# Performance work log

Measured on AMD Instinct MI355X. Metric: run time of the kernel, lower is better.

The kernel has to match this reference:

```python
import jax, jax.numpy as jnp
import numpy as np

D_MODEL = 512
NUM_HEADS = 8
WINDOW = 10
DEPTH = D_MODEL // NUM_HEADS


def positional_encoding(position, d_model):
    pos = np.arange(position)[:, None].astype(np.float32)
    i = np.arange(d_model)[None, :].astype(np.float32)
    angle = pos / np.power(10000.0, 2.0 * (np.floor(i / 2.0)) / np.float32(d_model))
    angle[:, 0::2] = np.sin(angle[:, 0::2])
    angle[:, 1::2] = np.cos(angle[:, 1::2])
    return jnp.asarray(angle[None, ...], dtype=jnp.float32)  # [1, n, d_model]


def forward(x, wq_w, wq_b, wk_w, wk_b, wv_w, wv_b, dense_w, dense_b):
    B, C, S, _ = x.shape
    data = x[..., 0]
    mask = x[..., 2]
    data = data.reshape(B, C, -1, WINDOW)   # [B,C,n,W]
    mask = mask.reshape(B, C, -1, WINDOW)
    n = data.shape[2]

    # mean_module: (data*mask).mean over window, drop first/last window
    mean_feature = jnp.mean(data * mask, axis=-1, keepdims=True)[:, :, 1:-1]  # [B,C,n-2,1]

    # combined look-ahead + padding mask
    mask_min = jnp.min(mask[:, :, 1:-1], axis=-1)              # [B,C,n-2]
    n2 = n - 2
    look_ahead = 1.0 - jnp.tril(jnp.ones((n2, n2), jnp.float32))
    padding = (mask_min == 0).astype(jnp.float32)[:, :, None, None, :]  # [B,C,1,1,n-2]
    comb_mask = jnp.maximum(look_ahead, padding)               # [B,C,1,n-2,n-2]

    # positional encoding over window dimension
    pe = positional_encoding(n, WINDOW)                        # [1,n,W]
    data = data + pe[None]                                     # [B,C,n,W]

    # q,k from concatenated future/past windows; v from current windows
    qk_in = jnp.concatenate([data[:, :, 2:], data[:, :, :-2]], axis=-1)  # [B,C,n-2,2W]
    q = qk_in @ wq_w + wq_b
    k = qk_in @ wk_w + wk_b
    v = data[:, :, 1:-1] @ wv_w + wv_b                          # [B,C,n-2,d_model]

    def split_heads(t):
        return t.reshape(B, C, n2, NUM_HEADS, DEPTH).transpose(0, 1, 3, 2, 4)

    q, k, v = split_heads(q), split_heads(k), split_heads(v)    # [B,C,H,n-2,depth]

    logits = jnp.einsum('bchqd,bchkd->bchqk', q, k) / jnp.sqrt(jnp.float32(DEPTH))
    logits = logits + comb_mask * (-1e9)
    attn = jax.nn.softmax(logits, axis=-1)
    ctx = jnp.einsum('bchqk,bchkd->bchqd', attn, v)
    ctx = ctx.transpose(0, 1, 3, 2, 4).reshape(B, C, n2, D_MODEL)

    concat = jnp.concatenate([ctx, mean_feature], axis=-1)      # [B,C,n-2,d_model+1]
    out = concat @ dense_w + dense_b                            # [B,C,n-2,W]
    return out.reshape(B, C, -1)[..., None]                     # [B,C,(n-2)*W,1]


def setup_inputs() -> dict:
    key = jax.random.key(0)
    ks = jax.random.split(key, 8)
    B, C, S = 16, 16, 2560
    data = jax.random.normal(ks[0], (B, C, S), jnp.float32)
    time = jnp.zeros((B, C, S), jnp.float32)
    mask = (jax.random.uniform(ks[1], (B, C, S)) < 0.9).astype(jnp.float32)
    x = jnp.stack([data, time, mask], axis=-1)
    scale = 0.02
    return {
        'x': x,
        'wq_w': jax.random.normal(ks[2], (2 * WINDOW, D_MODEL), jnp.float32) * scale,
        'wq_b': jnp.zeros((D_MODEL,), jnp.float32),
        'wk_w': jax.random.normal(ks[3], (2 * WINDOW, D_MODEL), jnp.float32) * scale,
        'wk_b': jnp.zeros((D_MODEL,), jnp.float32),
        'wv_w': jax.random.normal(ks[4], (WINDOW, D_MODEL), jnp.float32) * scale,
        'wv_b': jnp.zeros((D_MODEL,), jnp.float32),
        'dense_w': jax.random.normal(ks[5], (D_MODEL + 1, WINDOW), jnp.float32) * scale,
        'dense_b': jnp.zeros((WINDOW,), jnp.float32),
    }


def reference(x, wq_w, wq_b, wk_w, wk_b, wv_w, wv_b, dense_w, dense_b):
    return forward(x, wq_w, wq_b, wk_w, wk_b, wv_w, wv_b, dense_w, dense_b)
```

## Files before the change

kernel.cpp:

```cpp
#include <hip/hip_runtime.h>

#define LOG2E 1.44269504088896340736f
#define SCL 0.18033688011111772f

typedef __bf16 bf16x8 __attribute__((ext_vector_type(8)));
typedef float f32x16 __attribute__((ext_vector_type(16)));

union U4B { uint4 u; bf16x8 v; };

static __device__ __forceinline__ unsigned short f2bf(float f) {
  unsigned u = __builtin_bit_cast(unsigned, f);
  u += 0x7FFFu + ((u >> 16) & 1u);
  return (unsigned short)(u >> 16);
}
static __device__ __forceinline__ float bf2f(unsigned short s) {
  unsigned u = ((unsigned)s) << 16;
  return __builtin_bit_cast(float, u);
}
static __device__ __forceinline__ f32x16 zero16() {
  f32x16 z;
#pragma unroll
  for (int i = 0; i < 16; ++i) z[i] = 0.f;
  return z;
}
static __device__ __forceinline__ f32x16 MFMA(bf16x8 a, bf16x8 b, f32x16 c) {
  return __builtin_amdgcn_mfma_f32_32x32x16_bf16(a, b, c, 0, 0, 0);
}

static __device__ __forceinline__ void xform(f32x16 t, int hi, uint4& f0, uint4& f1) {
  unsigned pk[8], sw[8];
#pragma unroll
  for (int s = 0; s < 8; ++s) {
    unsigned d;
    asm("v_cvt_pk_bf16_f32 %0, %1, %2" : "=v"(d) : "v"(t[2*s]), "v"(t[2*s+1]));
    pk[s] = d;
  }
#pragma unroll
  for (int s = 0; s < 8; ++s) sw[s] = (unsigned)__shfl_xor((int)pk[s], 32);
  if (hi) {
    f0 = make_uint4(sw[2], sw[3], pk[2], pk[3]);
    f1 = make_uint4(sw[6], sw[7], pk[6], pk[7]);
  } else {
    f0 = make_uint4(pk[0], pk[1], sw[0], sw[1]);
    f1 = make_uint4(pk[4], pk[5], sw[4], sw[5]);
  }
}

__global__ void zero_out_k(float* __restrict__ out, int n) {
  int i = blockIdx.x * 256 + threadIdx.x;
  if (i < n) out[i] = 0.f;
}

__global__ void setup_k(
    const float* __restrict__ wq_w, const float* __restrict__ wq_b,
    const float* __restrict__ wk_w, const float* __restrict__ wk_b,
    const float* __restrict__ wv_w, const float* __restrict__ wv_b,
    const float* __restrict__ dense_w, float* __restrict__ ws)
{
  int gid = blockIdx.x*256 + threadIdx.x;
  float* pe = ws;
  unsigned short* wqT = (unsigned short*)(ws + 2560);
  unsigned short* wkT = (unsigned short*)(ws + 10752);
  float* WVD = ws + 18944;
  float* bvd = ws + 19744;
  if (gid < 2560) {
    int i = gid/10, t = gid%10;
    double ex = (double)(2*(t/2)) / 10.0;
    double ang = (double)i * pow(10000.0, -ex);
    pe[gid] = (float)((t & 1) ? cos(ang) : sin(ang));
  } else if (gid < 2560 + 16384) {
    int idx = gid - 2560;
    int hd = idx >> 5, t = idx & 31;
    float v = (t < 20) ? wq_w[t*512 + hd] : ((t == 20) ? wq_b[hd] : 0.f);
    wqT[idx] = f2bf(v);
  } else if (gid < 2560 + 32768) {
    int idx = gid - (2560 + 16384);
    int hd = idx >> 5, t = idx & 31;
    float v = (t < 20) ? wk_w[t*512 + hd] : ((t == 20) ? wk_b[hd] : 0.f);
    wkT[idx] = f2bf(v);
  } else if (gid < 2560 + 32768 + 800) {
    int idx = gid - (2560 + 32768);
    int h = idx/100, rem = idx%100, t = rem/10, w = rem%10;
    float s = 0.f;
    for (int d = 0; d < 64; ++d) s += wv_w[t*512 + h*64 + d] * dense_w[(h*64 + d)*10 + w];
    WVD[idx] = s;
  } else if (gid < 2560 + 32768 + 880) {
    int idx = gid - (2560 + 32768 + 800);
    int h = idx/10, w = idx%10;
    float s = 0.f;
    for (int d = 0; d < 64; ++d) s += wv_b[h*64 + d] * dense_w[(h*64 + d)*10 + w];
    bvd[idx] = s;
  }
}

__global__ __launch_bounds__(256, 1) void mha_fused(
    const float* __restrict__ x,
    const float* __restrict__ dense_w, const float* __restrict__ dense_b,
    const unsigned short* __restrict__ wqT, const unsigned short* __restrict__ wkT,
    const float* __restrict__ WVD, const float* __restrict__ bvd,
    const float* __restrict__ pe,
    float* __restrict__ out)
{
  __shared__ __align__(16) unsigned short qk_in[256*24];
  __shared__ __align__(16) unsigned short k_lds[256*64];
  __shared__ __align__(16) unsigned short vdT[16*256];
  __shared__ unsigned short mean_b[256];
  __shared__ unsigned long long padb[4];
  __shared__ float ddmean_s[10];

  const int tid = threadIdx.x;
  const int lane = tid & 63;
  const int wv = tid >> 6;
  const int hi = lane >> 5;
  const int cc = lane & 31;
  const int bc = blockIdx.x / 3;
  const int p3 = blockIdx.x - bc*3;
  const int hbase = p3*3;
  const int nh = (p3 == 2) ? 2 : 3;

  float ddr[10];
  {
    const float* xb = x + ((size_t)bc*2560 + tid*10)*3;
    float dat[10], msk[10];
#pragma unroll
    for (int t = 0; t < 10; ++t) { dat[t] = xb[3*t]; msk[t] = xb[3*t+2]; }
    float mean = 0.f, mm = msk[0];
#pragma unroll
    for (int t = 0; t < 10; ++t) { mean += dat[t]*msk[t]; mm = fminf(mm, msk[t]); }
    mean_b[tid] = f2bf(mean * 0.1f);
    const float* per = pe + tid*10;
#pragma unroll
    for (int t = 0; t < 10; ++t) ddr[t] = dat[t] + per[t];
    float* ddtmp = (float*)k_lds;
    float* mmv = ddtmp + 2560;
#pragma unroll
    for (int t = 0; t < 10; ++t) ddtmp[tid*10 + t] = ddr[t];
    mmv[tid] = mm;
  }
  __syncthreads();
  {
    const float* ddtmp = (const float*)k_lds;
    const float* mmv = ddtmp + 2560;
    float* part = (float*)vdT;
    if (tid < 254) {
#pragma unroll
      for (int t = 0; t < 10; ++t) qk_in[tid*24 + t] = f2bf(ddtmp[(tid+2)*10 + t]);
#pragma unroll
      for (int t = 0; t < 10; ++t) qk_in[tid*24 + 10 + t] = f2bf(ddr[t]);
      qk_in[tid*24 + 20] = 0x3F80;
      qk_in[tid*24 + 21] = 0; qk_in[tid*24 + 22] = 0; qk_in[tid*24 + 23] = 0;
    } else {
#pragma unroll
      for (int t = 0; t < 24; ++t) qk_in[tid*24 + t] = 0;
    }
    if (tid < 160) {
      int t = tid >> 4, j = tid & 15;
      int w0 = 1 + j*16, w1 = (w0 + 16 < 255) ? (w0 + 16) : 255;
      float s = 0.f;
      for (int w = w0; w < w1; ++w) s += ddtmp[w*10 + t];
      part[tid] = s;
    }
#pragma unroll
    for (int i = 0; i < 6; ++i) vdT[(10 + i)*256 + tid] = 0;
    bool cond = (tid >= 254) || (mmv[tid+1] == 0.0f);
    unsigned long long bl = __ballot(cond);
    if (lane == 0) padb[wv] = bl;
  }
  __syncthreads();
  if (tid < 10) {
    const float* part = (const float*)vdT;
    float s = 0.f;
#pragma unroll
    for (int j = 0; j < 16; ++j) s += part[tid*16 + j];
    ddmean_s[tid] = s * (1.0f/254.0f);
  }
  float dwcol = 0.f, dbias = 0.f;
  if (cc < 10) { dwcol = dense_w[5120 + cc]; dbias = dense_b[cc]; }
  const unsigned* pw = (const unsigned*)padb;

  f32x16 outacc0 = zero16(), outacc1 = zero16();

#pragma unroll 1
  for (int hh = 0; hh < nh; ++hh) {
    const int h = hbase + hh;
    __syncthreads();
    if (tid < 254) {
      float df[10];
      int src = tid + 1;
      if (src <= 253) {
#pragma unroll
        for (int t = 0; t < 10; ++t) df[t] = bf2f(qk_in[src*24 + 10 + t]);
      } else {
#pragma unroll
        for (int t = 0; t < 10; ++t) df[t] = bf2f(qk_in[252*24 + t]);
      }
      const float* wvd = WVD + h*100;
      const float* bv = bvd + h*10;
#pragma unroll
      for (int w = 0; w < 10; ++w) {
        float s = bv[w];
#pragma unroll
        for (int t = 0; t < 10; ++t) s += df[t]*wvd[t*10 + w];
        vdT[w*256 + (tid ^ ((w & 15)*8))] = f2bf(s);
      }
    }
    if (tid < 32) {
      int w = tid >> 1, j = 254 + (tid & 1);
      vdT[w*256 + (j ^ ((w & 15)*8))] = 0;
    }
    float mvd = 0.f;
    if (cc < 10) {
      mvd = bvd[h*10 + cc];
#pragma unroll
      for (int t = 0; t < 10; ++t) mvd = fmaf(ddmean_s[t], WVD[h*100 + t*10 + cc], mvd);
    }
    __syncthreads();

#pragma unroll
    for (int jti = 0; jti < 2; ++jti) {
      int jt = wv + 4*jti;
      int krow = 32*jt + cc;
      U4B b0, b1;
      b0.u = *(const uint4*)&qk_in[krow*24 + 8*hi];
      b1.u = make_uint4(0,0,0,0);
      if (!hi) b1.u = *(const uint4*)&qk_in[krow*24 + 16];
#pragma unroll
      for (int it = 0; it < 2; ++it) {
        const unsigned short* wrow = wkT + (h*64 + 32*it + cc)*32;
        U4B a0, a1;
        a0.u = *(const uint4*)&wrow[8*hi];
        a1.u = *(const uint4*)&wrow[16 + 8*hi];
        f32x16 acc = zero16();
        acc = MFMA(a0.v, b0.v, acc);
        acc = MFMA(a1.v, b1.v, acc);
        uint4 f0, f1;
        xform(acc, hi, f0, f1);
        int dc0 = 2*it, dc1 = 2*it + 1;
        *(uint4*)&k_lds[krow*64 + ((8*(2*dc0 + hi)) ^ (8*(krow & 7)))] = f0;
        *(uint4*)&k_lds[krow*64 + ((8*(2*dc1 + hi)) ^ (8*(krow & 7)))] = f1;
      }
    }
    __syncthreads();

#pragma unroll
    for (int qti = 0; qti < 2; ++qti) {
      const int qt = qti ? (7 - wv) : wv;
      const int qrow = 32*qt + cc;
      uint4 qf0, qf1, qf2, qf3;
      {
        U4B b0, b1;
        b0.u = *(const uint4*)&qk_in[qrow*24 + 8*hi];
        b1.u = make_uint4(0,0,0,0);
        if (!hi) b1.u = *(const uint4*)&qk_in[qrow*24 + 16];
        {
          const unsigned short* wrow = wqT + (h*64 + cc)*32;
          U4B a0, a1;
          a0.u = *(const uint4*)&wrow[8*hi];
          a1.u = *(const uint4*)&wrow[16 + 8*hi];
          f32x16 acc = zero16();
          acc = MFMA(a0.v, b0.v, acc);
          acc = MFMA(a1.v, b1.v, acc);
          xform(acc, hi, qf0, qf1);
        }
        {
          const unsigned short* wrow = wqT + (h*64 + 32 + cc)*32;
          U4B a0, a1;
          a0.u = *(const uint4*)&wrow[8*hi];
          a1.u = *(const uint4*)&wrow[16 + 8*hi];
          f32x16 acc = zero16();
          acc = MFMA(a0.v, b0.v, acc);
          acc = MFMA(a1.v, b1.v, acc);
          xform(acc, hi, qf2, qf3);
        }
      }
      float sum = 0.f;
      f32x16 pv = zero16();
      const int vrow = cc & 15;
      const int vsw = 8*vrow;
#pragma unroll
      for (int kt = 0; kt < 8; ++kt) {
        if (kt <= qt) {
          const int kr = 32*kt + cc;
          const int kbase = kr*64;
          const int ksw = 8*(kr & 7);
          f32x16 a = zero16();
          U4B ka, qa;
          ka.u = *(const uint4*)&k_lds[kbase + ((8*(0 + hi)) ^ ksw)];
          qa.u = qf0; a = MFMA(ka.v, qa.v, a);
          ka.u = *(const uint4*)&k_lds[kbase + ((8*(2 + hi)) ^ ksw)];
          qa.u = qf1; a = MFMA(ka.v, qa.v, a);
          ka.u = *(const uint4*)&k_lds[kbase + ((8*(4 + hi)) ^ ksw)];
          qa.u = qf2; a = MFMA(ka.v, qa.v, a);
          ka.u = *(const uint4*)&k_lds[kbase + ((8*(6 + hi)) ^ ksw)];
          qa.u = qf3; a = MFMA(ka.v, qa.v, a);
          const unsigned pbk = pw[kt];
          if (kt < qt) {
#pragma unroll
            for (int r = 0; r < 16; ++r) {
              const int base = (r & 3) + 8*(r >> 2);
              const int pos = base + 4*hi;
              float add = ((pbk >> pos) & 1u) ? -2.0e9f : 0.0f;
              float p = exp2f(fmaf(a[r], SCL, add));
              a[r] = p;
              sum += p;
            }
          } else {
#pragma unroll
            for (int r = 0; r < 16; ++r) {
              const int base = (r & 3) + 8*(r >> 2);
              const int pos = base + 4*hi;
              bool mk = (((pbk >> pos) & 1u) != 0u) || (pos > cc);
              float add = mk ? -2.0e9f : 0.0f;
              float p = exp2f(fmaf(a[r], SCL, add));
              a[r] = p;
              sum += p;
            }
          }
          uint4 pa0, pa1;
          xform(a, hi, pa0, pa1);
          U4B pA, vB;
          pA.u = pa0;
          vB.u = *(const uint4*)&vdT[vrow*256 + ((32*kt + 8*hi) ^ vsw)];
          pv = MFMA(pA.v, vB.v, pv);
          pA.u = pa1;
          vB.u = *(const uint4*)&vdT[vrow*256 + ((32*kt + 16 + 8*hi) ^ vsw)];
          pv = MFMA(pA.v, vB.v, pv);
        }
      }
      float stot = sum + __shfl_xor(sum, 32);
      const float rs = 1.0f / fmaxf(stot, 1e-30f);
      bool pre = true;
#pragma unroll
      for (int j = 0; j < 8; ++j) { if (j < qt) pre = pre && (pw[j] == 0xFFFFFFFFu); }
      const unsigned pbq = pw[qt];
#pragma unroll
      for (int r = 0; r < 16; ++r) {
        const int base = (r & 3) + 8*(r >> 2);
        const int qr = base + 4*hi;
        unsigned lm = (qr == 31) ? 0xFFFFFFFFu : ((2u << qr) - 1u);
        bool degq = pre && ((pbq & lm) == lm);
        float rr = __shfl(rs, qr, 32);
        float contrib = degq ? mvd : pv[r]*rr;
        if (qti == 0) outacc0[r] += contrib; else outacc1[r] += contrib;
      }
    }
  }

#pragma unroll
  for (int qti = 0; qti < 2; ++qti) {
    const int qt = qti ? (7 - wv) : wv;
#pragma unroll
    for (int r = 0; r < 16; ++r) {
      const int base = (r & 3) + 8*(r >> 2);
      int q = 32*qt + base + 4*hi;
      if (q < 254 && cc < 10) {
        float v = (qti == 0 ? outacc0[r] : outacc1[r]);
        if (p3 == 0) v += bf2f(mean_b[q + 1])*dwcol + dbias;
        atomicAdd(&out[((size_t)bc*254 + q)*10 + cc], v);
      }
    }
  }
}

extern "C" void kernel_launch(void* const* d_in, const int* in_sizes, int n_in,
                              void* d_out, int out_size, void* d_ws, size_t ws_size,
                              hipStream_t stream) {
  const float* x       = (const float*)d_in[0];
  const float* wq_w    = (const float*)d_in[1];
  const float* wq_b    = (const float*)d_in[2];
  const float* wk_w    = (const float*)d_in[3];
  const float* wk_b    = (const float*)d_in[4];
  const float* wv_w    = (const float*)d_in[5];
  const float* wv_b    = (const float*)d_in[6];
  const float* dense_w = (const float*)d_in[7];
  const float* dense_b = (const float*)d_in[8];
  float* ws = (float*)d_ws;

  zero_out_k<<<(out_size + 255)/256, 256, 0, stream>>>((float*)d_out, out_size);
  setup_k<<<142, 256, 0, stream>>>(wq_w, wq_b, wk_w, wk_b, wv_w, wv_b, dense_w, ws);
  mha_fused<<<768, 256, 0, stream>>>(
      x, dense_w, dense_b,
      (const unsigned short*)(ws + 2560),
      (const unsigned short*)(ws + 10752),
      ws + 18944,
      ws + 19744,
      ws,
      (float*)d_out);
}
```

Baseline: 201.7 us.

## Recompute K projection in registers per tile instead of staging in LDS

Removes the k_lds shared buffer and the separate K-projection phase with its barrier. Each wave now recomputes the K fragments via MFMA for every key tile inside the attention loop, keeping the wk weights in registers. The qk_in window data is rebuilt from global x and pe rather than from an LDS float staging area, and the window-mean partial sums now read the bf16 values. This cuts LDS footprint and one sync per head, at the cost of redundant K MFMA work (each key tile recomputed by several waves), slightly lower precision in the mean, and more register pressure.

```diff
diff --git a/kernel.cpp b/kernel.cpp
--- a/kernel.cpp
+++ b/kernel.cpp
@@ -102,7 +102,6 @@
     float* __restrict__ out)
 {
   __shared__ __align__(16) unsigned short qk_in[256*24];
-  __shared__ __align__(16) unsigned short k_lds[256*64];
   __shared__ __align__(16) unsigned short vdT[16*256];
   __shared__ unsigned short mean_b[256];
   __shared__ unsigned long long padb[4];
@@ -131,20 +130,17 @@
     const float* per = pe + tid*10;
 #pragma unroll
     for (int t = 0; t < 10; ++t) ddr[t] = dat[t] + per[t];
-    float* ddtmp = (float*)k_lds;
-    float* mmv = ddtmp + 2560;
-#pragma unroll
-    for (int t = 0; t < 10; ++t) ddtmp[tid*10 + t] = ddr[t];
+    float* mmv = (float*)&vdT[512];
     mmv[tid] = mm;
   }
   __syncthreads();
   {
-    const float* ddtmp = (const float*)k_lds;
-    const float* mmv = ddtmp + 2560;
-    float* part = (float*)vdT;
+    const float* mmv = (const float*)&vdT[512];
     if (tid < 254) {
-#pragma unroll
-      for (int t = 0; t < 10; ++t) qk_in[tid*24 + t] = f2bf(ddtmp[(tid+2)*10 + t]);
+      const float* xb2 = x + ((size_t)bc*2560 + (tid+2)*10)*3;
+      const float* per2 = pe + (tid+2)*10;
+#pragma unroll
+      for (int t = 0; t < 10; ++t) qk_in[tid*24 + t] = f2bf(xb2[3*t] + per2[t]);
 #pragma unroll
       for (int t = 0; t < 10; ++t) qk_in[tid*24 + 10 + t] = f2bf(ddr[t]);
       qk_in[tid*24 + 20] = 0x3F80;
@@ -153,18 +149,23 @@
 #pragma unroll
       for (int t = 0; t < 24; ++t) qk_in[tid*24 + t] = 0;
     }
+#pragma unroll
+    for (int i = 0; i < 6; ++i) vdT[(10 + i)*256 + tid] = 0;
+    bool cond = (tid >= 254) || (mmv[tid+1] == 0.0f);
+    unsigned long long bl = __ballot(cond);
+    if (lane == 0) padb[wv] = bl;
+  }
+  __syncthreads();
+  {
+    float* part = (float*)vdT;
     if (tid < 160) {
       int t = tid >> 4, j = tid & 15;
       int w0 = 1 + j*16, w1 = (w0 + 16 < 255) ? (w0 + 16) : 255;
       float s = 0.f;
-      for (int w = w0; w < w1; ++w) s += ddtmp[w*10 + t];
+      for (int w = w0; w < w1; ++w)
+        s += (w < 254) ? bf2f(qk_in[w*24 + 10 + t]) : bf2f(qk_in[252*24 + t]);
       part[tid] = s;
     }
-#pragma unroll
-    for (int i = 0; i < 6; ++i) vdT[(10 + i)*256 + tid] = 0;
-    bool cond = (tid >= 254) || (mmv[tid+1] == 0.0f);
-    unsigned long long bl = __ballot(cond);
-    if (lane == 0) padb[wv] = bl;
   }
   __syncthreads();
   if (tid < 10) {
@@ -204,7 +205,7 @@
         vdT[w*256 + (tid ^ ((w & 15)*8))] = f2bf(s);
       }
     }
-    if (tid < 32) {
+    if (tid < 20) {
       int w = tid >> 1, j = 254 + (tid & 1);
       vdT[w*256 + (j ^ ((w & 15)*8))] = 0;
     }
@@ -216,31 +217,11 @@
     }
     __syncthreads();
 
-#pragma unroll
-    for (int jti = 0; jti < 2; ++jti) {
-      int jt = wv + 4*jti;
-      int krow = 32*jt + cc;
-      U4B b0, b1;
-      b0.u = *(const uint4*)&qk_in[krow*24 + 8*hi];
-      b1.u = make_uint4(0,0,0,0);
-      if (!hi) b1.u = *(const uint4*)&qk_in[krow*24 + 16];
-#pragma unroll
-      for (int it = 0; it < 2; ++it) {
-        const unsigned short* wrow = wkT + (h*64 + 32*it + cc)*32;
-        U4B a0, a1;
-        a0.u = *(const uint4*)&wrow[8*hi];
-        a1.u = *(const uint4*)&wrow[16 + 8*hi];
-        f32x16 acc = zero16();
-        acc = MFMA(a0.v, b0.v, acc);
-        acc = MFMA(a1.v, b1.v, acc);
-        uint4 f0, f1;
-        xform(acc, hi, f0, f1);
-        int dc0 = 2*it, dc1 = 2*it + 1;
-        *(uint4*)&k_lds[krow*64 + ((8*(2*dc0 + hi)) ^ (8*(krow & 7)))] = f0;
-        *(uint4*)&k_lds[krow*64 + ((8*(2*dc1 + hi)) ^ (8*(krow & 7)))] = f1;
-      }
-    }
-    __syncthreads();
+    U4B wk00, wk01, wk10, wk11;
+    wk00.u = *(const uint4*)&wkT[(h*64 + cc)*32 + 8*hi];
+    wk01.u = *(const uint4*)&wkT[(h*64 + cc)*32 + 16 + 8*hi];
+    wk10.u = *(const uint4*)&wkT[(h*64 + 32 + cc)*32 + 8*hi];
+    wk11.u = *(const uint4*)&wkT[(h*64 + 32 + cc)*32 + 16 + 8*hi];
 
 #pragma unroll
     for (int qti = 0; qti < 2; ++qti) {
@@ -281,18 +262,29 @@
       for (int kt = 0; kt < 8; ++kt) {
         if (kt <= qt) {
           const int kr = 32*kt + cc;
-          const int kbase = kr*64;
-          const int ksw = 8*(kr & 7);
+          U4B kb0, kb1;
+          kb0.u = *(const uint4*)&qk_in[kr*24 + 8*hi];
+          kb1.u = make_uint4(0,0,0,0);
+          if (!hi) kb1.u = *(const uint4*)&qk_in[kr*24 + 16];
+          uint4 kf0, kf1, kf2, kf3;
+          {
+            f32x16 acc = zero16();
+            acc = MFMA(wk00.v, kb0.v, acc);
+            acc = MFMA(wk01.v, kb1.v, acc);
+            xform(acc, hi, kf0, kf1);
+          }
+          {
+            f32x16 acc = zero16();
+            acc = MFMA(wk10.v, kb0.v, acc);
+            acc = MFMA(wk11.v, kb1.v, acc);
+            xform(acc, hi, kf2, kf3);
+          }
           f32x16 a = zero16();
           U4B ka, qa;
-          ka.u = *(const uint4*)&k_lds[kbase + ((8*(0 + hi)) ^ ksw)];
-          qa.u = qf0; a = MFMA(ka.v, qa.v, a);
-          ka.u = *(const uint4*)&k_lds[kbase + ((8*(2 + hi)) ^ ksw)];
-          qa.u = qf1; a = MFMA(ka.v, qa.v, a);
-          ka.u = *(const uint4*)&k_lds[kbase + ((8*(4 + hi)) ^ ksw)];
-          qa.u = qf2; a = MFMA(ka.v, qa.v, a);
-          ka.u = *(const uint4*)&k_lds[kbase + ((8*(6 + hi)) ^ ksw)];
-          qa.u = qf3; a = MFMA(ka.v, qa.v, a);
+          ka.u = kf0; qa.u = qf0; a = MFMA(ka.v, qa.v, a);
+          ka.u = kf1; qa.u = qf1; a = MFMA(ka.v, qa.v, a);
+          ka.u = kf2; qa.u = qf2; a = MFMA(ka.v, qa.v, a);
+          ka.u = kf3; qa.u = qf3; a = MFMA(ka.v, qa.v, a);
           const unsigned pbk = pw[kt];
           if (kt < qt) {
 #pragma unroll
```

Result: slower. 217.3 us (+7.7%).
